# Optimization experiments

Hardware: AMD Instinct MI355X
Metric: run time of the kernel (lower is better)

Reference implementation:

```python
import jax, jax.numpy as jnp
import numpy as np

B = 1024
IN = 512      # in_features
O = 64        # out_features
E = 8         # ensamble
K = O * E     # total tiny MLPs, index k = i*E + j (i: output, j: ensemble)


def setup_inputs() -> dict:
    key = jax.random.key(0)
    k1, k2, k3, k4, k5 = jax.random.split(key, 5)
    s = 1.0 / np.sqrt(IN)
    X = jax.random.normal(k1, (B, IN), dtype=jnp.float32)
    # Stacked weights for all K = O*E tiny MLPs.
    # nn.Linear(in,in): y = x @ W1^T + b1, W1: [in_out, in_in]
    W1 = jax.random.uniform(k2, (K, IN, IN), jnp.float32, -s, s)
    b1 = jax.random.uniform(k3, (K, IN), jnp.float32, -s, s)
    # nn.Linear(in,1): W2 squeezed to [K, IN], b2 to [K]
    W2 = jax.random.uniform(k4, (K, IN), jnp.float32, -s, s)
    b2 = jax.random.uniform(k5, (K,), jnp.float32, -s, s)
    return {"X": X, "W1": W1, "b1": b1, "W2": W2, "b2": b2}


def reference(X, W1, b1, W2, b2):
    # h[b,k,:] = relu(X[b] @ W1[k].T + b1[k])  -- one batched GEMM
    h = jax.nn.relu(jnp.einsum('bi,kji->bkj', X, W1) + b1)  # [B,K,IN]
    out = jnp.einsum('bkj,kj->bk', h, W2) + b2              # [B,K]
    # original: concat over ensemble (dim=-1) then stack over out_features (dim=-1)
    out = out.reshape(X.shape[0], O, E).transpose(0, 2, 1)  # [B,E,O]
    return out
```

## Files before the change

kernel.cpp:

```cpp
#include <hip/hip_runtime.h>
#include <hip/hip_bf16.h>

typedef __attribute__((ext_vector_type(8))) short short8;
typedef __attribute__((ext_vector_type(4))) float f32x4;

__device__ __forceinline__ short8 pack8(const f32x4& a, const f32x4& b) {
    union { __hip_bfloat162 h[4]; short8 s; } u;
    u.h[0] = __float22bfloat162_rn(make_float2(a[0], a[1]));
    u.h[1] = __float22bfloat162_rn(make_float2(a[2], a[3]));
    u.h[2] = __float22bfloat162_rn(make_float2(b[0], b[1]));
    u.h[3] = __float22bfloat162_rn(make_float2(b[2], b[3]));
    return u.s;
}

__device__ __forceinline__ int swz(int g) { return g ^ (((g >> 4) & 3) << 4 >> 3); }
__device__ __forceinline__ int swz4(int g) { return g ^ (((g >> 4) & 3) << 1); }


#define ISSUE(S, BASE, KT1)                                                   \
  do {                                                                        \
    const float* q_ = (BASE) + (KT1) * 64;                                    \
    S[0] = *(const f32x4*)q_;          S[1] = *(const f32x4*)(q_ + 4);        \
    S[2] = *(const f32x4*)(q_ + 32);   S[3] = *(const f32x4*)(q_ + 36);       \
    const float* q2_ = q_ + 65536;                                            \
    S[4] = *(const f32x4*)q2_;         S[5] = *(const f32x4*)(q2_ + 4);       \
    S[6] = *(const f32x4*)(q2_ + 32);  S[7] = *(const f32x4*)(q2_ + 36);      \
  } while (0)

#define WRITEB(S, WB, OPOFF)                                                  \
  do {                                                                        \
    char* d0_ = (WB) + (OPOFF) + wfrag;                                       \
    *(short8*)d0_ = pack8(S[0], S[1]);                                        \
    *(short8*)(d0_ + 1024) = pack8(S[2], S[3]);                               \
    char* d1_ = d0_ + 16384;                                                  \
    *(short8*)d1_ = pack8(S[4], S[5]);                                        \
    *(short8*)(d1_ + 1024) = pack8(S[6], S[7]);                               \
  } while (0)

#define KK(RB, KKV)                                                           \
  do {                                                                        \
    _Pragma("unroll") for (int mi = 0; mi < 8; ++mi)                          \
        av[mi] = *(const short8*)((RB) +                                      \
            (((wm * 8 + mi) * 2 + (KKV)) << 10) + rdo);                       \
    _Pragma("unroll") for (int pp = 0; pp < 4; ++pp)                          \
        bv[pp] = *(const short8*)((RB) + 32768 +                              \
            (((wn * 4 + pp) * 2 + (KKV)) << 10) + rdo);                       \
    __builtin_amdgcn_s_setprio(1);                                            \
    _Pragma("unroll") for (int mi = 0; mi < 8; ++mi)                          \
        _Pragma("unroll") for (int pp = 0; pp < 4; ++pp)                      \
            acc[mi][pp] = __builtin_amdgcn_mfma_f32_16x16x32_bf16(            \
                av[mi], bv[pp], acc[mi][pp], 0, 0, 0);                        \
    __builtin_amdgcn_s_setprio(0);                                            \
  } while (0)

#define PRO_WRITE(TT, ROFF)                                                   \
  do {                                                                        \
    short8 a_ = pack8(TT[0], TT[1]);                                          \
    short8 b_ = pack8(TT[2], TT[3]);                                          \
    char* d_ = smem + (ROFF) + wfrag;                                         \
    *(short8*)d_ = a_;                                                        \
    *(short8*)(d_ + 1024) = b_;                                               \
  } while (0)

__global__ __launch_bounds__(512, 2)
void ens_mlp_kernel(const float* __restrict__ X,
                    const float* __restrict__ W1,
                    const float* __restrict__ B1,
                    const float* __restrict__ W2,
                    const float* __restrict__ B2,
                    float* __restrict__ out)
{
    extern __shared__ char smem[];
    const int t    = threadIdx.x;
    const int lane = t & 63;
    const int wv   = t >> 6;
    const int wm   = wv >> 2;
    const int wn   = wv & 3;

    const int bb  = blockIdx.x;
    const int xcd = bb & 7;
    const int j   = bb >> 3;
    const int km  = xcd * 64 + (j >> 3);
    const int sub = j & 7;
    const int mt  = sub >> 1;
    const int nt  = sub & 1;

    const float* __restrict__ W1k = W1 + (size_t)km * (512 * 512);

    const int lr = t >> 2;
    const int c  = t & 3;
    const float* As = X   + (size_t)(mt * 256 + lr) * 512 + c * 8;
    const float* Bs = W1k + (size_t)(nt * 256 + lr) * 512 + c * 8;
    const int wfrag = ((lr >> 4) << 11) + (swz4((c << 4) | (lr & 15)) << 4);
    const int rdo   = swz4(lane) << 4;

    {
        f32x4 t0[4], t1[4], t2[4], t3[4];
        const float* q;
        q = As;          t0[0]=*(const f32x4*)q; t0[1]=*(const f32x4*)(q+4); t0[2]=*(const f32x4*)(q+32); t0[3]=*(const f32x4*)(q+36);
        q = As + 65536;  t1[0]=*(const f32x4*)q; t1[1]=*(const f32x4*)(q+4); t1[2]=*(const f32x4*)(q+32); t1[3]=*(const f32x4*)(q+36);
        q = Bs;          t2[0]=*(const f32x4*)q; t2[1]=*(const f32x4*)(q+4); t2[2]=*(const f32x4*)(q+32); t2[3]=*(const f32x4*)(q+36);
        q = Bs + 65536;  t3[0]=*(const f32x4*)q; t3[1]=*(const f32x4*)(q+4); t3[2]=*(const f32x4*)(q+32); t3[3]=*(const f32x4*)(q+36);
        asm volatile("s_waitcnt vmcnt(12)" ::: "memory"); PRO_WRITE(t0, 0);
        asm volatile("s_waitcnt vmcnt(8)"  ::: "memory"); PRO_WRITE(t1, 16384);
        asm volatile("s_waitcnt vmcnt(4)"  ::: "memory"); PRO_WRITE(t2, 32768);
        asm volatile("s_waitcnt vmcnt(0)"  ::: "memory"); PRO_WRITE(t3, 49152);
        asm volatile("s_waitcnt lgkmcnt(0)" ::: "memory");
        __builtin_amdgcn_sched_barrier(0);
        __builtin_amdgcn_s_barrier();
    }

    f32x4 acc[8][4];
#pragma unroll
    for (int i = 0; i < 8; ++i)
#pragma unroll
        for (int p = 0; p < 4; ++p)
            acc[i][p] = (f32x4)0.0f;

    short8 av[8], bv[4];
    f32x4 sS[8];

#pragma unroll 1
    for (int kt = 0; kt < 7; ++kt) {
        const char* rb = smem + (kt & 1) * 65536;
        char* wb       = smem + ((kt + 1) & 1) * 65536;

        ISSUE(sS, Bs, kt + 1);
        KK(rb, 0);
        asm volatile("s_waitcnt vmcnt(0)" ::: "memory");
        WRITEB(sS, wb, 32768);
        ISSUE(sS, As, kt + 1);
        KK(rb, 1);
        asm volatile("s_waitcnt vmcnt(0)" ::: "memory");
        WRITEB(sS, wb, 0);
        asm volatile("s_waitcnt lgkmcnt(0)" ::: "memory");
        __builtin_amdgcn_sched_barrier(0);
        __builtin_amdgcn_s_barrier();
    }
    {
        const char* rb = smem + 65536;
        KK(rb, 0);
        KK(rb, 1);
    }

    const int nc = lane & 15;
    const int kq = lane >> 4;
    float b1v[4], w2v[4];
#pragma unroll
    for (int pp = 0; pp < 4; ++pp) {
        int n = nt * 256 + (wn * 4 + pp) * 16 + nc;
        b1v[pp] = B1[km * 512 + n];
        w2v[pp] = W2[km * 512 + n];
    }

    float* lout = (float*)smem;
#pragma unroll
    for (int i = 0; i < 8; ++i) {
#pragma unroll
        for (int r = 0; r < 4; ++r) {
            float s = 0.f;
#pragma unroll
            for (int pp = 0; pp < 4; ++pp) {
                float h = acc[i][pp][r] + b1v[pp];
                h = h > 0.f ? h : 0.f;
                s += h * w2v[pp];
            }
#pragma unroll
            for (int d = 1; d < 16; d <<= 1)
                s += __shfl_xor(s, d, 64);
            if (nc == 0) {
                int row = wm * 128 + i * 16 + kq * 4 + r;
                lout[row * 4 + wn] = s;
            }
        }
    }
    __syncthreads();
    if (t < 256) {
        float s = lout[t * 4 + 0] + lout[t * 4 + 1] + lout[t * 4 + 2] + lout[t * 4 + 3];
        if (nt == 0) s += B2[km];
        int b = mt * 256 + t;
        atomicAdd(out + (size_t)b * 512 + (km & 7) * 64 + (km >> 3), s);
    }
}

extern "C" void kernel_launch(void* const* d_in, const int* in_sizes, int n_in,
                              void* d_out, int out_size, void* d_ws, size_t ws_size,
                              hipStream_t stream) {
    const float* X  = (const float*)d_in[0];
    const float* W1 = (const float*)d_in[1];
    const float* B1 = (const float*)d_in[2];
    const float* W2 = (const float*)d_in[3];
    const float* B2 = (const float*)d_in[4];
    float* out = (float*)d_out;

    hipMemsetAsync(out, 0, (size_t)out_size * sizeof(float), stream);
    ens_mlp_kernel<<<dim3(4096), dim3(512), 131072, stream>>>(X, W1, B1, W2, B2, out);
}
```

Measured before the change: 428.2 us.

## Shrink GEMM tile to 256x128 with 4 waves and single-stage K=32 pipeline

```diff
diff --git a/kernel.cpp b/kernel.cpp
--- a/kernel.cpp
+++ b/kernel.cpp
@@ -13,38 +13,33 @@
     return u.s;
 }
 
-__device__ __forceinline__ int swz(int g) { return g ^ (((g >> 4) & 3) << 4 >> 3); }
 __device__ __forceinline__ int swz4(int g) { return g ^ (((g >> 4) & 3) << 1); }
 
+#define BUF 24576
 
-#define ISSUE(S, BASE, KT1)                                                   \
+#define ISSUE_B(KT1)                                                          \
   do {                                                                        \
-    const float* q_ = (BASE) + (KT1) * 64;                                    \
-    S[0] = *(const f32x4*)q_;          S[1] = *(const f32x4*)(q_ + 4);        \
-    S[2] = *(const f32x4*)(q_ + 32);   S[3] = *(const f32x4*)(q_ + 36);       \
-    const float* q2_ = q_ + 65536;                                            \
-    S[4] = *(const f32x4*)q2_;         S[5] = *(const f32x4*)(q2_ + 4);       \
-    S[6] = *(const f32x4*)(q2_ + 32);  S[7] = *(const f32x4*)(q2_ + 36);      \
+    const float* q_ = Bs + (KT1) * 32;                                        \
+    sB[0] = *(const f32x4*)q_;           sB[1] = *(const f32x4*)(q_ + 4);     \
+    sB[2] = *(const f32x4*)(q_ + 32768); sB[3] = *(const f32x4*)(q_ + 32772); \
   } while (0)
 
-#define WRITEB(S, WB, OPOFF)                                                  \
+#define ISSUE_A(KT1)                                                          \
   do {                                                                        \
-    char* d0_ = (WB) + (OPOFF) + wfrag;                                       \
-    *(short8*)d0_ = pack8(S[0], S[1]);                                        \
-    *(short8*)(d0_ + 1024) = pack8(S[2], S[3]);                               \
-    char* d1_ = d0_ + 16384;                                                  \
-    *(short8*)d1_ = pack8(S[4], S[5]);                                        \
-    *(short8*)(d1_ + 1024) = pack8(S[6], S[7]);                               \
+    const float* q_ = As + (KT1) * 32;                                        \
+    sA[0] = *(const f32x4*)q_;           sA[1] = *(const f32x4*)(q_ + 4);     \
+    sA[2] = *(const f32x4*)(q_ + 32768); sA[3] = *(const f32x4*)(q_ + 32772); \
+    sA[4] = *(const f32x4*)(q_ + 65536); sA[5] = *(const f32x4*)(q_ + 65540); \
+    sA[6] = *(const f32x4*)(q_ + 98304); sA[7] = *(const f32x4*)(q_ + 98308); \
   } while (0)
 
-#define KK(RB, KKV)                                                           \
+#define KK(RB)                                                                \
   do {                                                                        \
     _Pragma("unroll") for (int mi = 0; mi < 8; ++mi)                          \
-        av[mi] = *(const short8*)((RB) +                                      \
-            (((wm * 8 + mi) * 2 + (KKV)) << 10) + rdo);                       \
+        av[mi] = *(const short8*)((RB) + ((wm * 8 + mi) << 10) + rdo);        \
     _Pragma("unroll") for (int pp = 0; pp < 4; ++pp)                          \
-        bv[pp] = *(const short8*)((RB) + 32768 +                              \
-            (((wn * 4 + pp) * 2 + (KKV)) << 10) + rdo);                       \
+        bv[pp] = *(const short8*)((RB) + 16384 +                              \
+                                  ((wn * 4 + pp) << 10) + rdo);               \
     __builtin_amdgcn_s_setprio(1);                                            \
     _Pragma("unroll") for (int mi = 0; mi < 8; ++mi)                          \
         _Pragma("unroll") for (int pp = 0; pp < 4; ++pp)                      \
@@ -53,16 +48,19 @@
     __builtin_amdgcn_s_setprio(0);                                            \
   } while (0)
 
-#define PRO_WRITE(TT, ROFF)                                                   \
+#define WRITE_ALL(WB)                                                         \
   do {                                                                        \
-    short8 a_ = pack8(TT[0], TT[1]);                                          \
-    short8 b_ = pack8(TT[2], TT[3]);                                          \
-    char* d_ = smem + (ROFF) + wfrag;                                         \
-    *(short8*)d_ = a_;                                                        \
-    *(short8*)(d_ + 1024) = b_;                                               \
+    char* db_ = (WB) + 16384 + wfrag;                                         \
+    *(short8*)db_ = pack8(sB[0], sB[1]);                                      \
+    *(short8*)(db_ + 4096) = pack8(sB[2], sB[3]);                             \
+    char* da_ = (WB) + wfrag;                                                 \
+    *(short8*)da_ = pack8(sA[0], sA[1]);                                      \
+    *(short8*)(da_ + 4096) = pack8(sA[2], sA[3]);                             \
+    *(short8*)(da_ + 8192) = pack8(sA[4], sA[5]);                             \
+    *(short8*)(da_ + 12288) = pack8(sA[6], sA[7]);                            \
   } while (0)
 
-__global__ __launch_bounds__(512, 2)
+__global__ __launch_bounds__(256, 2)
 void ens_mlp_kernel(const float* __restrict__ X,
                     const float* __restrict__ W1,
                     const float* __restrict__ B1,
@@ -74,37 +72,43 @@
     const int t    = threadIdx.x;
     const int lane = t & 63;
     const int wv   = t >> 6;
-    const int wm   = wv >> 2;
-    const int wn   = wv & 3;
+    const int wm   = wv >> 1;
+    const int wn   = wv & 1;
 
     const int bb  = blockIdx.x;
     const int xcd = bb & 7;
     const int j   = bb >> 3;
-    const int km  = xcd * 64 + (j >> 3);
-    const int sub = j & 7;
-    const int mt  = sub >> 1;
-    const int nt  = sub & 1;
+    const int km  = xcd * 64 + (j >> 4);
+    const int sub = j & 15;
+    const int mt  = sub >> 2;
+    const int ntq = sub & 3;
 
     const float* __restrict__ W1k = W1 + (size_t)km * (512 * 512);
 
     const int lr = t >> 2;
     const int c  = t & 3;
     const float* As = X   + (size_t)(mt * 256 + lr) * 512 + c * 8;
-    const float* Bs = W1k + (size_t)(nt * 256 + lr) * 512 + c * 8;
-    const int wfrag = ((lr >> 4) << 11) + (swz4((c << 4) | (lr & 15)) << 4);
+    const float* Bs = W1k + (size_t)(ntq * 128 + lr) * 512 + c * 8;
+    const int wfrag = ((lr >> 4) << 10) + (swz4((c << 4) | (lr & 15)) << 4);
     const int rdo   = swz4(lane) << 4;
 
+    f32x4 sB[4], sA[8];
+
     {
-        f32x4 t0[4], t1[4], t2[4], t3[4];
-        const float* q;
-        q = As;          t0[0]=*(const f32x4*)q; t0[1]=*(const f32x4*)(q+4); t0[2]=*(const f32x4*)(q+32); t0[3]=*(const f32x4*)(q+36);
-        q = As + 65536;  t1[0]=*(const f32x4*)q; t1[1]=*(const f32x4*)(q+4); t1[2]=*(const f32x4*)(q+32); t1[3]=*(const f32x4*)(q+36);
-        q = Bs;          t2[0]=*(const f32x4*)q; t2[1]=*(const f32x4*)(q+4); t2[2]=*(const f32x4*)(q+32); t2[3]=*(const f32x4*)(q+36);
-        q = Bs + 65536;  t3[0]=*(const f32x4*)q; t3[1]=*(const f32x4*)(q+4); t3[2]=*(const f32x4*)(q+32); t3[3]=*(const f32x4*)(q+36);
-        asm volatile("s_waitcnt vmcnt(12)" ::: "memory"); PRO_WRITE(t0, 0);
-        asm volatile("s_waitcnt vmcnt(8)"  ::: "memory"); PRO_WRITE(t1, 16384);
-        asm volatile("s_waitcnt vmcnt(4)"  ::: "memory"); PRO_WRITE(t2, 32768);
-        asm volatile("s_waitcnt vmcnt(0)"  ::: "memory"); PRO_WRITE(t3, 49152);
+        ISSUE_B(0);
+        ISSUE_A(0);
+        asm volatile("s_waitcnt vmcnt(8)" ::: "memory");
+        { char* d = smem + 16384 + wfrag;
+          *(short8*)d = pack8(sB[0], sB[1]);
+          *(short8*)(d + 4096) = pack8(sB[2], sB[3]); }
+        asm volatile("s_waitcnt vmcnt(4)" ::: "memory");
+        { char* d = smem + wfrag;
+          *(short8*)d = pack8(sA[0], sA[1]);
+          *(short8*)(d + 4096) = pack8(sA[2], sA[3]); }
+        asm volatile("s_waitcnt vmcnt(0)" ::: "memory");
+        { char* d = smem + wfrag;
+          *(short8*)(d + 8192)  = pack8(sA[4], sA[5]);
+          *(short8*)(d + 12288) = pack8(sA[6], sA[7]); }
         asm volatile("s_waitcnt lgkmcnt(0)" ::: "memory");
         __builtin_amdgcn_sched_barrier(0);
         __builtin_amdgcn_s_barrier();
@@ -118,29 +122,25 @@
             acc[i][p] = (f32x4)0.0f;
 
     short8 av[8], bv[4];
-    f32x4 sS[8];
 
 #pragma unroll 1
-    for (int kt = 0; kt < 7; ++kt) {
-        const char* rb = smem + (kt & 1) * 65536;
-        char* wb       = smem + ((kt + 1) & 1) * 65536;
+    for (int kt = 0; kt < 15; ++kt) {
+        const char* rb = smem + (kt & 1) * BUF;
+        char* wb       = smem + ((kt + 1) & 1) * BUF;
 
-        ISSUE(sS, Bs, kt + 1);
-        KK(rb, 0);
+        ISSUE_B(kt + 1);
+        ISSUE_A(kt + 1);
+        __builtin_amdgcn_sched_barrier(0);
+        KK(rb);
         asm volatile("s_waitcnt vmcnt(0)" ::: "memory");
-        WRITEB(sS, wb, 32768);
-        ISSUE(sS, As, kt + 1);
-        KK(rb, 1);
-        asm volatile("s_waitcnt vmcnt(0)" ::: "memory");
-        WRITEB(sS, wb, 0);
+        WRITE_ALL(wb);
         asm volatile("s_waitcnt lgkmcnt(0)" ::: "memory");
         __builtin_amdgcn_sched_barrier(0);
         __builtin_amdgcn_s_barrier();
     }
     {
-        const char* rb = smem + 65536;
-        KK(rb, 0);
-        KK(rb, 1);
+        const char* rb = smem + BUF;
+        KK(rb);
     }
 
     const int nc = lane & 15;
@@ -148,7 +148,7 @@
     float b1v[4], w2v[4];
 #pragma unroll
     for (int pp = 0; pp < 4; ++pp) {
-        int n = nt * 256 + (wn * 4 + pp) * 16 + nc;
+        int n = ntq * 128 + (wn * 4 + pp) * 16 + nc;
         b1v[pp] = B1[km * 512 + n];
         w2v[pp] = W2[km * 512 + n];
     }
@@ -170,14 +170,14 @@
                 s += __shfl_xor(s, d, 64);
             if (nc == 0) {
                 int row = wm * 128 + i * 16 + kq * 4 + r;
-                lout[row * 4 + wn] = s;
+                lout[row * 2 + wn] = s;
             }
         }
     }
     __syncthreads();
-    if (t < 256) {
-        float s = lout[t * 4 + 0] + lout[t * 4 + 1] + lout[t * 4 + 2] + lout[t * 4 + 3];
-        if (nt == 0) s += B2[km];
+    {
+        float s = lout[t * 2 + 0] + lout[t * 2 + 1];
+        if (ntq == 0) s += B2[km];
         int b = mt * 256 + t;
         atomicAdd(out + (size_t)b * 512 + (km & 7) * 64 + (km >> 3), s);
     }
@@ -194,5 +194,5 @@
     float* out = (float*)d_out;
 
     hipMemsetAsync(out, 0, (size_t)out_size * sizeof(float), stream);
-    ens_mlp_kernel<<<dim3(4096), dim3(512), 131072, stream>>>(X, W1, B1, W2, B2, out);
+    ens_mlp_kernel<<<dim3(8192), dim3(256), 2 * BUF, stream>>>(X, W1, B1, W2, B2, out);
 }
```

New measurement: 488.7 us. 14.1% more time.

## Pre-convert X and W1 to bf16 fragments, then stream them via global_load_lds

Applied to the files above, without the earlier changes.

```diff
diff --git a/kernel.cpp b/kernel.cpp
--- a/kernel.cpp
+++ b/kernel.cpp
@@ -13,11 +13,171 @@
     return u.s;
 }
 
-__device__ __forceinline__ int swz(int g) { return g ^ (((g >> 4) & 3) << 4 >> 3); }
 __device__ __forceinline__ int swz4(int g) { return g ^ (((g >> 4) & 3) << 1); }
 
-
-#define ISSUE(S, BASE, KT1)                                                   \
+#define GLDS(GP, LP)                                                          \
+    __builtin_amdgcn_global_load_lds(                                         \
+        (__attribute__((address_space(1))) void*)(void*)(GP),                 \
+        (__attribute__((address_space(3))) void*)(void*)(LP), 16, 0, 0)
+
+__global__ __launch_bounds__(256)
+void ens_cvt(const float* __restrict__ X, const float* __restrict__ W1,
+             short* __restrict__ WS)
+{
+    const int t = threadIdx.x, lane = t & 63, wv = t >> 6;
+    const int g = blockIdx.x * 4 + wv;
+    const int row16 = lane & 15, koct = lane >> 4;
+    const float* src;
+    short* dst;
+    if (blockIdx.x < 4096) {
+        const int km = g >> 5, f = g & 31;
+        src = W1 + (size_t)km * 262144 + (size_t)(f * 16 + row16) * 512 + koct * 8;
+        dst = WS + (size_t)km * 262144 + (size_t)(f * 16) * 512 + lane * 8;
+    } else {
+        const int mf = g - 16384;
+        src = X + (size_t)(mf * 16 + row16) * 512 + koct * 8;
+        dst = WS + 134217728ull + (size_t)(mf * 16) * 512 + lane * 8;
+    }
+#pragma unroll
+    for (int ks = 0; ks < 16; ++ks) {
+        f32x4 a = *(const f32x4*)(src + ks * 32);
+        f32x4 b = *(const f32x4*)(src + ks * 32 + 4);
+        *(short8*)(dst + ks * 512) = pack8(a, b);
+    }
+}
+
+#define ISSUE(H)                                                              \
+  do {                                                                        \
+    char* sb_ = smem + ((H) & 3) * 32768;                                     \
+    GLDS(g0 + (H) * 512, sb_ + (size_t)(s0 + 0) * 1024);                      \
+    GLDS(g1 + (H) * 512, sb_ + (size_t)(s0 + 1) * 1024);                      \
+    GLDS(g2 + (H) * 512, sb_ + (size_t)(s0 + 2) * 1024);                      \
+    GLDS(g3 + (H) * 512, sb_ + (size_t)(s0 + 3) * 1024);                      \
+  } while (0)
+
+#define KK(H)                                                                 \
+  do {                                                                        \
+    const char* rb_ = smem + ((H) & 3) * 32768;                               \
+    _Pragma("unroll") for (int mi = 0; mi < 8; ++mi)                          \
+        av[mi] = *(const short8*)(rb_ + (wm * 8 + mi) * 1024 + (lane << 4));  \
+    _Pragma("unroll") for (int pp = 0; pp < 4; ++pp)                          \
+        bv[pp] = *(const short8*)(rb_ + 16384 +                               \
+                                  (wn * 4 + pp) * 1024 + (lane << 4));        \
+    __builtin_amdgcn_s_setprio(1);                                            \
+    _Pragma("unroll") for (int mi = 0; mi < 8; ++mi)                          \
+        _Pragma("unroll") for (int pp = 0; pp < 4; ++pp)                      \
+            acc[mi][pp] = __builtin_amdgcn_mfma_f32_16x16x32_bf16(            \
+                av[mi], bv[pp], acc[mi][pp], 0, 0, 0);                        \
+    __builtin_amdgcn_s_setprio(0);                                            \
+  } while (0)
+
+__global__ __launch_bounds__(512, 2)
+void ens_gemm_dma(const short* __restrict__ Xb, const short* __restrict__ W1b,
+                  const float* __restrict__ B1, const float* __restrict__ W2,
+                  const float* __restrict__ B2, float* __restrict__ out)
+{
+    extern __shared__ char smem[];
+    const int t    = threadIdx.x;
+    const int lane = t & 63;
+    const int wv   = t >> 6;
+    const int wm   = wv >> 2;
+    const int wn   = wv & 3;
+
+    const int bb  = blockIdx.x;
+    const int xcd = bb & 7;
+    const int j   = bb >> 3;
+    const int km  = xcd * 64 + (j >> 3);
+    const int sub = j & 7;
+    const int mt  = sub >> 1;
+    const int nt  = sub & 1;
+
+    const int s0 = wv * 4;
+    const short* g0;
+    const short* g1;
+    const short* g2;
+    const short* g3;
+    {
+        auto gsrc = [&](int s) -> const short* {
+            if (s < 16)
+                return Xb + (size_t)(mt * 16 + s) * 16 * 512 + lane * 8;
+            return W1b + (size_t)km * 262144 +
+                   (size_t)(nt * 16 + (s - 16)) * 16 * 512 + lane * 8;
+        };
+        g0 = gsrc(s0); g1 = gsrc(s0 + 1); g2 = gsrc(s0 + 2); g3 = gsrc(s0 + 3);
+    }
+
+    f32x4 acc[8][4];
+#pragma unroll
+    for (int i = 0; i < 8; ++i)
+#pragma unroll
+        for (int p = 0; p < 4; ++p)
+            acc[i][p] = (f32x4)0.0f;
+
+    short8 av[8], bv[4];
+
+    ISSUE(0);
+    ISSUE(1);
+    ISSUE(2);
+    asm volatile("s_waitcnt vmcnt(8)" ::: "memory");
+    __builtin_amdgcn_sched_barrier(0);
+    __builtin_amdgcn_s_barrier();
+    __builtin_amdgcn_sched_barrier(0);
+
+#pragma unroll 1
+    for (int h = 0; h < 16; ++h) {
+        if (h < 13) ISSUE(h + 3);
+        KK(h);
+        if (h < 13)       asm volatile("s_waitcnt vmcnt(8)" ::: "memory");
+        else if (h == 13) asm volatile("s_waitcnt vmcnt(4)" ::: "memory");
+        else if (h == 14) asm volatile("s_waitcnt vmcnt(0)" ::: "memory");
+        if (h < 15) {
+            __builtin_amdgcn_sched_barrier(0);
+            __builtin_amdgcn_s_barrier();
+            __builtin_amdgcn_sched_barrier(0);
+        }
+    }
+
+    const int nc = lane & 15;
+    const int kq = lane >> 4;
+    float b1v[4], w2v[4];
+#pragma unroll
+    for (int pp = 0; pp < 4; ++pp) {
+        int n = nt * 256 + (wn * 4 + pp) * 16 + nc;
+        b1v[pp] = B1[km * 512 + n];
+        w2v[pp] = W2[km * 512 + n];
+    }
+
+    float* lout = (float*)smem;
+#pragma unroll
+    for (int i = 0; i < 8; ++i) {
+#pragma unroll
+        for (int r = 0; r < 4; ++r) {
+            float s = 0.f;
+#pragma unroll
+            for (int pp = 0; pp < 4; ++pp) {
+                float h = acc[i][pp][r] + b1v[pp];
+                h = h > 0.f ? h : 0.f;
+                s += h * w2v[pp];
+            }
+#pragma unroll
+            for (int d = 1; d < 16; d <<= 1)
+                s += __shfl_xor(s, d, 64);
+            if (nc == 0) {
+                int row = wm * 128 + i * 16 + kq * 4 + r;
+                lout[row * 4 + wn] = s;
+            }
+        }
+    }
+    __syncthreads();
+    if (t < 256) {
+        float s = lout[t * 4 + 0] + lout[t * 4 + 1] + lout[t * 4 + 2] + lout[t * 4 + 3];
+        if (nt == 0) s += B2[km];
+        int b = mt * 256 + t;
+        atomicAdd(out + (size_t)b * 512 + (km & 7) * 64 + (km >> 3), s);
+    }
+}
+
+#define FISSUE(S, BASE, KT1)                                                  \
   do {                                                                        \
     const float* q_ = (BASE) + (KT1) * 64;                                    \
     S[0] = *(const f32x4*)q_;          S[1] = *(const f32x4*)(q_ + 4);        \
@@ -27,7 +187,7 @@
     S[6] = *(const f32x4*)(q2_ + 32);  S[7] = *(const f32x4*)(q2_ + 36);      \
   } while (0)
 
-#define WRITEB(S, WB, OPOFF)                                                  \
+#define FWRITEB(S, WB, OPOFF)                                                 \
   do {                                                                        \
     char* d0_ = (WB) + (OPOFF) + wfrag;                                       \
     *(short8*)d0_ = pack8(S[0], S[1]);                                        \
@@ -37,7 +197,7 @@
     *(short8*)(d1_ + 1024) = pack8(S[6], S[7]);                               \
   } while (0)
 
-#define KK(RB, KKV)                                                           \
+#define FKK(RB, KKV)                                                          \
   do {                                                                        \
     _Pragma("unroll") for (int mi = 0; mi < 8; ++mi)                          \
         av[mi] = *(const short8*)((RB) +                                      \
@@ -53,7 +213,7 @@
     __builtin_amdgcn_s_setprio(0);                                            \
   } while (0)
 
-#define PRO_WRITE(TT, ROFF)                                                   \
+#define FPRO_WRITE(TT, ROFF)                                                  \
   do {                                                                        \
     short8 a_ = pack8(TT[0], TT[1]);                                          \
     short8 b_ = pack8(TT[2], TT[3]);                                          \
@@ -63,12 +223,12 @@
   } while (0)
 
 __global__ __launch_bounds__(512, 2)
-void ens_mlp_kernel(const float* __restrict__ X,
-                    const float* __restrict__ W1,
-                    const float* __restrict__ B1,
-                    const float* __restrict__ W2,
-                    const float* __restrict__ B2,
-                    float* __restrict__ out)
+void ens_mlp_fallback(const float* __restrict__ X,
+                      const float* __restrict__ W1,
+                      const float* __restrict__ B1,
+                      const float* __restrict__ W2,
+                      const float* __restrict__ B2,
+                      float* __restrict__ out)
 {
     extern __shared__ char smem[];
     const int t    = threadIdx.x;
@@ -101,10 +261,10 @@
         q = As + 65536;  t1[0]=*(const f32x4*)q; t1[1]=*(const f32x4*)(q+4); t1[2]=*(const f32x4*)(q+32); t1[3]=*(const f32x4*)(q+36);
         q = Bs;          t2[0]=*(const f32x4*)q; t2[1]=*(const f32x4*)(q+4); t2[2]=*(const f32x4*)(q+32); t2[3]=*(const f32x4*)(q+36);
         q = Bs + 65536;  t3[0]=*(const f32x4*)q; t3[1]=*(const f32x4*)(q+4); t3[2]=*(const f32x4*)(q+32); t3[3]=*(const f32x4*)(q+36);
-        asm volatile("s_waitcnt vmcnt(12)" ::: "memory"); PRO_WRITE(t0, 0);
-        asm volatile("s_waitcnt vmcnt(8)"  ::: "memory"); PRO_WRITE(t1, 16384);
-        asm volatile("s_waitcnt vmcnt(4)"  ::: "memory"); PRO_WRITE(t2, 32768);
-        asm volatile("s_waitcnt vmcnt(0)"  ::: "memory"); PRO_WRITE(t3, 49152);
+        asm volatile("s_waitcnt vmcnt(12)" ::: "memory"); FPRO_WRITE(t0, 0);
+        asm volatile("s_waitcnt vmcnt(8)"  ::: "memory"); FPRO_WRITE(t1, 16384);
+        asm volatile("s_waitcnt vmcnt(4)"  ::: "memory"); FPRO_WRITE(t2, 32768);
+        asm volatile("s_waitcnt vmcnt(0)"  ::: "memory"); FPRO_WRITE(t3, 49152);
         asm volatile("s_waitcnt lgkmcnt(0)" ::: "memory");
         __builtin_amdgcn_sched_barrier(0);
         __builtin_amdgcn_s_barrier();
@@ -125,22 +285,22 @@
         const char* rb = smem + (kt & 1) * 65536;
         char* wb       = smem + ((kt + 1) & 1) * 65536;
 
-        ISSUE(sS, Bs, kt + 1);
-        KK(rb, 0);
+        FISSUE(sS, Bs, kt + 1);
+        FKK(rb, 0);
         asm volatile("s_waitcnt vmcnt(0)" ::: "memory");
-        WRITEB(sS, wb, 32768);
-        ISSUE(sS, As, kt + 1);
-        KK(rb, 1);
+        FWRITEB(sS, wb, 32768);
+        FISSUE(sS, As, kt + 1);
+        FKK(rb, 1);
         asm volatile("s_waitcnt vmcnt(0)" ::: "memory");
-        WRITEB(sS, wb, 0);
+        FWRITEB(sS, wb, 0);
         asm volatile("s_waitcnt lgkmcnt(0)" ::: "memory");
         __builtin_amdgcn_sched_barrier(0);
         __builtin_amdgcn_s_barrier();
     }
     {
         const char* rb = smem + 65536;
-        KK(rb, 0);
-        KK(rb, 1);
+        FKK(rb, 0);
+        FKK(rb, 1);
     }
 
     const int nc = lane & 15;
@@ -194,5 +354,15 @@
     float* out = (float*)d_out;
 
     hipMemsetAsync(out, 0, (size_t)out_size * sizeof(float), stream);
-    ens_mlp_kernel<<<dim3(4096), dim3(512), 131072, stream>>>(X, W1, B1, W2, B2, out);
-}
+
+    const size_t NEED = 269484032ull;
+    if (ws_size >= NEED) {
+        short* WS = (short*)d_ws;
+        ens_cvt<<<dim3(4112), dim3(256), 0, stream>>>(X, W1, WS);
+        ens_gemm_dma<<<dim3(4096), dim3(512), 131072, stream>>>(
+            WS + 134217728ull, WS, B1, W2, B2, out);
+    } else {
+        ens_mlp_fallback<<<dim3(4096), dim3(512), 131072, stream>>>(
+            X, W1, B1, W2, B2, out);
+    }
+}
```

After: 470.2 us. +9.8%, slower.
